# Kernel tuning notes

Measured on AMD Instinct MI355X. Metric: run time of the kernel, lower is better.

## Reference

```python
import jax, jax.numpy as jnp
import numpy as np

B, S, DM = 2, 2048, 1024  # batch, seq_len, model_dim
H, HD = 16, 64            # num_heads, head_dim (H*HD == DM)


def setup_inputs() -> dict:
    key = jax.random.key(0)
    ks = jax.random.split(key, 8)
    scale = 0.02
    return {
        "k": jax.random.normal(ks[0], (B, S, DM), jnp.float32),
        "q": jax.random.normal(ks[1], (B, S, DM), jnp.float32),
        "v": jax.random.normal(ks[2], (B, S, DM), jnp.float32),
        "Wk": jax.random.normal(ks[3], (DM, H * HD), jnp.float32) * scale,
        "bk": jnp.zeros((H * HD,), jnp.float32),
        "Wq": jax.random.normal(ks[4], (DM, H * HD), jnp.float32) * scale,
        "bq": jnp.zeros((H * HD,), jnp.float32),
        "Wv": jax.random.normal(ks[5], (DM, H * HD), jnp.float32) * scale,
        "bv": jnp.zeros((H * HD,), jnp.float32),
        "Wo": jax.random.normal(ks[6], (H * HD, DM), jnp.float32) * scale,
        "bo": jnp.zeros((DM,), jnp.float32),
    }


def reference(k, q, v, Wk, bk, Wq, bq, Wv, bv, Wo, bo):
    # QKV projections (Dense with bias)
    kp = (k @ Wk + bk).reshape(B, S, H, HD)
    qp = (q @ Wq + bq).reshape(B, S, H, HD)
    vp = (v @ Wv + bv).reshape(B, S, H, HD)
    # Faithful to original: scores indexed [b, key_c, h, query_q],
    # softmax over the QUERY axis, NO 1/sqrt(head_dim) scaling.
    scores = jnp.einsum('bchd,bqhd->bchq', kp, qp)
    attn = jax.nn.softmax(scores, axis=-1)
    out = jnp.einsum('bchq,bqhd->bchd', attn, vp)  # [B, S(keys), H, HD]
    out = out.reshape(B, S, H * HD)
    return out @ Wo + bo
```

## Files before the change

### kernel.cpp

```cpp
#include <hip/hip_runtime.h>
#include <hip/hip_bf16.h>
#include <stdint.h>
#include <stddef.h>


typedef __attribute__((ext_vector_type(4))) float f32x4;
typedef __attribute__((ext_vector_type(16))) float f32x16;
typedef __attribute__((ext_vector_type(8))) short s16x8;
typedef __attribute__((ext_vector_type(4))) unsigned int u32x4;
typedef __attribute__((ext_vector_type(4))) unsigned short u16x4;

#define DEV static __device__ __forceinline__

DEV unsigned short f2bf(float x) {
  unsigned int u = __float_as_uint(x);
  u += 0x7FFF + ((u >> 16) & 1);
  return (unsigned short)(u >> 16);
}
DEV f32x4 mfma16(s16x8 a, s16x8 b, f32x4 c) {
  return __builtin_amdgcn_mfma_f32_16x16x32_bf16(a, b, c, 0, 0, 0);
}
DEV f32x16 mfma32(s16x8 a, s16x8 b, f32x16 c) {
  return __builtin_amdgcn_mfma_f32_32x32x16_bf16(a, b, c, 0, 0, 0);
}
DEV f32x4 fzero() { f32x4 z; z[0]=0.f; z[1]=0.f; z[2]=0.f; z[3]=0.f; return z; }
DEV f32x16 fzero16() {
  f32x16 z;
#pragma unroll
  for (int i = 0; i < 16; ++i) z[i] = 0.f;
  return z;
}
DEV float fexp2(float x) { return __builtin_amdgcn_exp2f(x); }

DEV void gload_lds16(const unsigned short* g, unsigned short* l) {
  __builtin_amdgcn_global_load_lds(
      (const __attribute__((address_space(1))) unsigned int*)g,
      (__attribute__((address_space(3))) unsigned int*)l, 16, 0, 0);
}

#define CVTPK(dst, a, b) \
  asm("v_cvt_pk_bf16_f32 %0, %1, %2" : "=v"(dst) : "v"(a), "v"(b))
#define PSWAP(x, y) \
  asm("v_permlane32_swap_b32 %0, %1" : "+v"(x), "+v"(y))

struct PrepArgs {
  const float* x[3]; unsigned short* y[3];
  const float* W[4]; unsigned short* Wt[4];
};

__global__ __launch_bounds__(256) void prep_kernel(PrepArgs a) {
  __shared__ float t[32][33];
  const int plane = blockIdx.y;
  if (plane < 3) {
    const float* x = a.x[plane];
    unsigned short* y = a.y[plane];
    const int i = blockIdx.x * 256 + threadIdx.x;
    f32x4 v0 = ((const f32x4*)x)[2*i];
    f32x4 v1 = ((const f32x4*)x)[2*i + 1];
    u16x4 o0, o1;
#pragma unroll
    for (int j = 0; j < 4; ++j) { o0[j] = f2bf(v0[j]); o1[j] = f2bf(v1[j]); }
    ((u16x4*)y)[2*i] = o0;
    ((u16x4*)y)[2*i + 1] = o1;
  } else {
    if (blockIdx.x >= 1024) return;
    const float* W = a.W[plane - 3];
    unsigned short* Wt = a.Wt[plane - 3];
    const int n0 = (blockIdx.x & 31) * 32, k0 = (blockIdx.x >> 5) * 32;
    const int tx = threadIdx.x & 31, ty = threadIdx.x >> 5;
#pragma unroll
    for (int i = 0; i < 4; ++i)
      t[ty + i*8][tx] = W[(size_t)(k0 + ty + i*8) * 1024 + n0 + tx];
    __syncthreads();
#pragma unroll
    for (int i = 0; i < 4; ++i)
      Wt[(size_t)(n0 + ty + i*8) * 1024 + k0 + tx] = f2bf(t[tx][ty + i*8]);
  }
}

struct GemArgs {
  const unsigned short* A[3];
  const unsigned short* Wt[3];
  const float* bias[3];
  void* C[3];
  int mode[3];
  float scale[3];
};

template<int BM, int BN>
__global__ __launch_bounds__(256) void gemm_kernel(GemArgs g) {
  constexpr int MF = BM / 32;
  constexpr int NF = BN / 32;
  constexpr int NB = BN / 32;
  const int z = blockIdx.z;
  const unsigned short* A  = g.A[z];
  const unsigned short* Wt = g.Wt[z];
  const float* bias = g.bias[z];
  const int mode = g.mode[z];
  const float scale = g.scale[z];
  const int Fb = blockIdx.y * gridDim.x + blockIdx.x;
  const int chunk = gridDim.y >> 3;
  const int myi = (Fb & 7) * chunk + ((Fb >> 3) % chunk);
  const int nxi = (Fb >> 3) / chunk;
  const int m0 = myi * BM, n0 = nxi * BN;
  const int tid = threadIdx.x;
  const int lane = tid & 63, w = tid >> 6;
  const int wm = w >> 1, wn = w & 1;
  const int lg = lane >> 4, lr = lane & 15, lx = lr & 7;

  __shared__ __align__(16) unsigned short As[BM * 64];
  __shared__ __align__(16) unsigned short Bs[BN * 64];

  f32x4 acc[MF][NF];
#pragma unroll
  for (int i = 0; i < MF; ++i)
#pragma unroll
    for (int j = 0; j < NF; ++j) acc[i][j] = fzero();

  const int aStep = (mode == 2) ? 2048 * 64 : 64;
  const unsigned short* srcA[MF]; unsigned short* dstA[MF];
#pragma unroll
  for (int c = 0; c < MF; ++c) {
    int n = c*256 + tid, row = n >> 3, cg = (n & 7) ^ (row & 7);
    int s = m0 + row;
    size_t abase = (mode == 2)
        ? ((size_t)((s >> 11) * 16) * 2048 + (s & 2047)) * 64 + cg * 8
        : (size_t)s * 1024 + cg * 8;
    srcA[c] = A + abase;
    dstA[c] = &As[n * 8];
  }
  const unsigned short* srcB[NB]; unsigned short* dstB[NB];
#pragma unroll
  for (int c = 0; c < NB; ++c) {
    int n = c*256 + tid, row = n >> 3, cg = (n & 7) ^ (row & 7);
    srcB[c] = Wt + (size_t)(n0 + row) * 1024 + cg * 8;
    dstB[c] = &Bs[n * 8];
  }

  for (int it = 0; it < 16; ++it) {
    __syncthreads();
#pragma unroll
    for (int c = 0; c < MF; ++c) { gload_lds16(srcA[c], dstA[c]); srcA[c] += aStep; }
#pragma unroll
    for (int c = 0; c < NB; ++c) { gload_lds16(srcB[c], dstB[c]); srcB[c] += 64; }
    __syncthreads();

    s16x8 af[2][MF], bf[2][NF];
#pragma unroll
    for (int ks = 0; ks < 2; ++ks) {
#pragma unroll
      for (int mf = 0; mf < MF; ++mf) {
        int row = wm*(BM/2) + mf*16 + lr;
        af[ks][mf] = *(const s16x8*)&As[row*64 + ((ks*4 + lg) ^ lx) * 8];
      }
#pragma unroll
      for (int nf = 0; nf < NF; ++nf) {
        int row = wn*(BN/2) + nf*16 + lr;
        bf[ks][nf] = *(const s16x8*)&Bs[row*64 + ((ks*4 + lg) ^ lx) * 8];
      }
    }
#pragma unroll
    for (int mf = 0; mf < MF; ++mf)
#pragma unroll
      for (int nf = 0; nf < NF; ++nf) {
        acc[mf][nf] = mfma16(af[0][mf], bf[0][nf], acc[mf][nf]);
        acc[mf][nf] = mfma16(af[1][mf], bf[1][nf], acc[mf][nf]);
      }
  }

#pragma unroll
  for (int nf = 0; nf < NF; ++nf) {
    const int colg = n0 + wn*(BN/2) + nf*16 + lr;
    const float bi = bias[colg];
#pragma unroll
    for (int mf = 0; mf < MF; ++mf) {
      const int rowg0 = m0 + wm*(BM/2) + mf*16 + lg*4;
      if (mode == 0) {
        unsigned short* o = (unsigned short*)g.C[z];
#pragma unroll
        for (int r = 0; r < 4; ++r)
          o[(size_t)(rowg0 + r) * 1024 + colg] = f2bf((acc[mf][nf][r] + bi) * scale);
      } else if (mode == 1) {
        const int hh = colg >> 6, d = colg & 63;
        const int bb2 = rowg0 >> 11, s = rowg0 & 2047;
        u16x4 pk;
#pragma unroll
        for (int r = 0; r < 4; ++r) pk[r] = f2bf(acc[mf][nf][r] + bi);
        *(u16x4*)((unsigned short*)g.C[z] + ((size_t)((bb2*16 + hh)*64 + d)) * 2048 + s) = pk;
      } else {
        float* o = (float*)g.C[z];
#pragma unroll
        for (int r = 0; r < 4; ++r)
          o[(size_t)(rowg0 + r) * 1024 + colg] = acc[mf][nf][r] + bi;
      }
    }
  }
}

__global__ __launch_bounds__(256) void attn_kernel(
    const unsigned short* __restrict__ kp, const unsigned short* __restrict__ qp,
    const unsigned short* __restrict__ vpt, unsigned short* __restrict__ aout) {
  const int F = blockIdx.x;
  const int swz = (F & 7) * 64 + (F >> 3);
  const int bh = swz >> 4, cblk = swz & 15;
  const int b = bh >> 4, h = bh & 15;
  const int c0 = cblk * 128;
  const int tid = threadIdx.x, lane = tid & 63, w = tid >> 6;
  const int cg = w & 1, jg = w >> 1;
  const int ln = lane & 31, hh = lane >> 5;

  __shared__ __align__(16) unsigned short qa_lds[2][2][2048];
  __shared__ __align__(16) unsigned short vb_lds[2][2][2048];
  __shared__ float lbuf[2][2][64];

  const int srow = tid >> 3, sp = tid & 7, sl = sp ^ (srow & 7);
  const unsigned short* qsrc0 =
      qp + (size_t)(b*2048 + srow) * 1024 + h*64 + sl*8;
  const unsigned short* qsrc1 = qsrc0 + (size_t)1024 * 1024;
  const int sd = srow + 32*(sl >> 2), sjc = sl & 3;
  const unsigned short* vsrc0 =
      vpt + ((size_t)((b*16 + h)*64) + sd) * 2048 + sjc*8;
  const unsigned short* vsrc1 = vsrc0 + 1024;

  s16x8 kbA[4], kbB[4];
  {
    const unsigned short* krowA =
        kp + (size_t)(b*2048 + c0 + cg*64 + ln) * 1024 + h*64 + hh*8;
    const unsigned short* krowB = krowA + 32 * 1024;
#pragma unroll
    for (int s = 0; s < 4; ++s) {
      kbA[s] = *(const s16x8*)(krowA + s*16);
      kbB[s] = *(const s16x8*)(krowB + s*16);
    }
  }

  s16x8 onesA, onesB;
  {
    const short oa = (short)((ln < 16) ? 0x3F80 : 0);
    const short ob = (short)((ln < 16) ? 0 : 0x3F80);
#pragma unroll
    for (int i = 0; i < 8; ++i) { onesA[i] = oa; onesB[i] = ob; }
  }

  f32x16 accA0 = fzero16(), accA1 = fzero16();
  f32x16 accB0 = fzero16(), accB1 = fzero16();
  f32x16 lacc = fzero16();

  gload_lds16(qsrc0, &qa_lds[0][0][tid*8]);
  gload_lds16(qsrc1, &qa_lds[0][1][tid*8]);
  gload_lds16(vsrc0, &vb_lds[0][0][tid*8]);
  gload_lds16(vsrc1, &vb_lds[0][1][tid*8]);
  qsrc0 += 32*1024; qsrc1 += 32*1024; vsrc0 += 32; vsrc1 += 32;
  __syncthreads();

  for (int jt = 0; jt < 32; ++jt) {
    const int cur = jt & 1;
    if (jt + 1 < 32) {
      gload_lds16(qsrc0, &qa_lds[cur^1][0][tid*8]);
      gload_lds16(qsrc1, &qa_lds[cur^1][1][tid*8]);
      gload_lds16(vsrc0, &vb_lds[cur^1][0][tid*8]);
      gload_lds16(vsrc1, &vb_lds[cur^1][1][tid*8]);
      qsrc0 += 32*1024; qsrc1 += 32*1024; vsrc0 += 32; vsrc1 += 32;
    }

    s16x8 qa0, qa1, qa2, qa3;
    {
      const unsigned short* base = &qa_lds[cur][jg][0];
      qa0 = *(const s16x8*)&base[(ln*8 + ((0 + hh) ^ (ln & 7)))*8];
      qa1 = *(const s16x8*)&base[(ln*8 + ((2 + hh) ^ (ln & 7)))*8];
      qa2 = *(const s16x8*)&base[(ln*8 + ((4 + hh) ^ (ln & 7)))*8];
      qa3 = *(const s16x8*)&base[(ln*8 + ((6 + hh) ^ (ln & 7)))*8];
    }
    s16x8 vb0, vb1, vb2, vb3;
    {
      const unsigned short* base = &vb_lds[cur][jg][0];
      vb0 = *(const s16x8*)&base[(ln*8 + ((0 + hh) ^ (ln & 7)))*8];
      vb1 = *(const s16x8*)&base[(ln*8 + ((2 + hh) ^ (ln & 7)))*8];
      vb2 = *(const s16x8*)&base[(ln*8 + ((4 + hh) ^ (ln & 7)))*8];
      vb3 = *(const s16x8*)&base[(ln*8 + ((6 + hh) ^ (ln & 7)))*8];
    }

    f32x16 scA = fzero16(), scB = fzero16();
    __builtin_amdgcn_s_setprio(1);
    scA = mfma32(qa0, kbA[0], scA); scA = mfma32(qa1, kbA[1], scA);
    scA = mfma32(qa2, kbA[2], scA); scA = mfma32(qa3, kbA[3], scA);
    scB = mfma32(qa0, kbB[0], scB); scB = mfma32(qa1, kbB[1], scB);
    scB = mfma32(qa2, kbB[2], scB); scB = mfma32(qa3, kbB[3], scB);
    __builtin_amdgcn_s_setprio(0);

#define SOFTMAX_PV(SC, ONES, ACC0, ACC1)                                      \
  {                                                                           \
    _Pragma("unroll")                                                         \
    for (int r = 0; r < 16; ++r) SC[r] = fexp2(SC[r]);                        \
    unsigned int a0, a1, b0, b1;                                              \
    u32x4 wv; s16x8 pa0, pa1;                                                 \
    CVTPK(a0, SC[0], SC[1]);  CVTPK(b0, SC[4], SC[5]);  PSWAP(a0, b0);        \
    CVTPK(a1, SC[2], SC[3]);  CVTPK(b1, SC[6], SC[7]);  PSWAP(a1, b1);        \
    wv[0] = a0; wv[1] = a1; wv[2] = b0; wv[3] = b1;                           \
    pa0 = __builtin_bit_cast(s16x8, wv);                                      \
    CVTPK(a0, SC[8], SC[9]);  CVTPK(b0, SC[12], SC[13]); PSWAP(a0, b0);       \
    CVTPK(a1, SC[10], SC[11]); CVTPK(b1, SC[14], SC[15]); PSWAP(a1, b1);      \
    wv[0] = a0; wv[1] = a1; wv[2] = b0; wv[3] = b1;                           \
    pa1 = __builtin_bit_cast(s16x8, wv);                                      \
    __builtin_amdgcn_s_setprio(1);                                            \
    lacc = mfma32(ONES, pa0, lacc);                                           \
    lacc = mfma32(ONES, pa1, lacc);                                           \
    ACC0 = mfma32(vb0, pa0, ACC0);                                            \
    ACC0 = mfma32(vb1, pa1, ACC0);                                            \
    ACC1 = mfma32(vb2, pa0, ACC1);                                            \
    ACC1 = mfma32(vb3, pa1, ACC1);                                            \
    __builtin_amdgcn_s_setprio(0);                                            \
  }

    SOFTMAX_PV(scA, onesA, accA0, accA1);
    SOFTMAX_PV(scB, onesB, accB0, accB1);
#undef SOFTMAX_PV

    __syncthreads();
  }

  float lA = lacc[0], lB = lacc[8];

  float* mrg = cg ? (float*)&vb_lds[0][0][0] : (float*)&qa_lds[0][0][0];
  if (jg == 1) {
    lbuf[cg][0][lane] = lA; lbuf[cg][1][lane] = lB;
#pragma unroll
    for (int r = 0; r < 16; ++r) {
      mrg[(r)*64 + lane]      = accA0[r];
      mrg[(16 + r)*64 + lane] = accA1[r];
      mrg[(32 + r)*64 + lane] = accB0[r];
      mrg[(48 + r)*64 + lane] = accB1[r];
    }
  }
  __syncthreads();
  if (jg == 0) {
    lA += lbuf[cg][0][lane]; lB += lbuf[cg][1][lane];
#pragma unroll
    for (int r = 0; r < 16; ++r) {
      accA0[r] += mrg[(r)*64 + lane];
      accA1[r] += mrg[(16 + r)*64 + lane];
      accB0[r] += mrg[(32 + r)*64 + lane];
      accB1[r] += mrg[(48 + r)*64 + lane];
    }
    const float invA = 1.0f / lA, invB = 1.0f / lB;
    unsigned short* obaseA =
        aout + ((size_t)bh * 2048 + c0 + cg*64 + ln) * 64 + hh * 4;
    unsigned short* obaseB = obaseA + 32 * 64;
#pragma unroll
    for (int dt = 0; dt < 2; ++dt)
#pragma unroll
      for (int rq = 0; rq < 4; ++rq) {
        u16x4 pkA, pkB;
#pragma unroll
        for (int i = 0; i < 4; ++i) {
          const int reg = rq*4 + i;
          pkA[i] = f2bf(((dt == 0) ? accA0[reg] : accA1[reg]) * invA);
          pkB[i] = f2bf(((dt == 0) ? accB0[reg] : accB1[reg]) * invB);
        }
        *(u16x4*)(obaseA + dt*32 + rq*8) = pkA;
        *(u16x4*)(obaseB + dt*32 + rq*8) = pkB;
      }
  }
}

extern "C" void kernel_launch(void* const* d_in, const int* in_sizes, int n_in,
                              void* d_out, int out_size, void* d_ws, size_t ws_size,
                              hipStream_t stream) {
  (void)in_sizes; (void)n_in; (void)out_size; (void)ws_size;
  const float* k  = (const float*)d_in[0];
  const float* q  = (const float*)d_in[1];
  const float* v  = (const float*)d_in[2];
  const float* Wk = (const float*)d_in[3];
  const float* bk = (const float*)d_in[4];
  const float* Wq = (const float*)d_in[5];
  const float* bq = (const float*)d_in[6];
  const float* Wv = (const float*)d_in[7];
  const float* bv = (const float*)d_in[8];
  const float* Wo = (const float*)d_in[9];
  const float* bo = (const float*)d_in[10];

  char* ws = (char*)d_ws;
  const size_t MB = 1024 * 1024;
  unsigned short* Wkt = (unsigned short*)(ws + 0*MB);
  unsigned short* Wqt = (unsigned short*)(ws + 2*MB);
  unsigned short* Wvt = (unsigned short*)(ws + 4*MB);
  unsigned short* Wot = (unsigned short*)(ws + 6*MB);
  unsigned short* kp  = (unsigned short*)(ws + 8*MB);
  unsigned short* qp  = (unsigned short*)(ws + 16*MB);
  unsigned short* vpt = (unsigned short*)(ws + 24*MB);
  unsigned short* vc  = (unsigned short*)(ws + 32*MB);
  unsigned short* aoutb = (unsigned short*)(ws + 40*MB);
  unsigned short* kc = (unsigned short*)d_out;
  unsigned short* qc = (unsigned short*)((char*)d_out + 8*MB);

  PrepArgs pa;
  pa.x[0] = k; pa.x[1] = q; pa.x[2] = v;
  pa.y[0] = kc; pa.y[1] = qc; pa.y[2] = vc;
  pa.W[0] = Wk; pa.W[1] = Wq; pa.W[2] = Wv; pa.W[3] = Wo;
  pa.Wt[0] = Wkt; pa.Wt[1] = Wqt; pa.Wt[2] = Wvt; pa.Wt[3] = Wot;
  prep_kernel<<<dim3(2048, 7), 256, 0, stream>>>(pa);

  GemArgs gp;
  gp.A[0] = kc; gp.A[1] = qc; gp.A[2] = vc;
  gp.Wt[0] = Wkt; gp.Wt[1] = Wqt; gp.Wt[2] = Wvt;
  gp.bias[0] = bk; gp.bias[1] = bq; gp.bias[2] = bv;
  gp.C[0] = kp; gp.C[1] = qp; gp.C[2] = vpt;
  gp.mode[0] = 0; gp.mode[1] = 0; gp.mode[2] = 1;
  gp.scale[0] = 1.4426950408889634f;
  gp.scale[1] = 1.0f; gp.scale[2] = 1.0f;
  gemm_kernel<128, 128><<<dim3(8, 32, 3), 256, 0, stream>>>(gp);

  attn_kernel<<<dim3(512), 256, 0, stream>>>(kp, qp, vpt, aoutb);

  GemArgs gf;
  gf.A[0] = aoutb; gf.A[1] = aoutb; gf.A[2] = aoutb;
  gf.Wt[0] = Wot; gf.Wt[1] = Wot; gf.Wt[2] = Wot;
  gf.bias[0] = bo; gf.bias[1] = bo; gf.bias[2] = bo;
  gf.C[0] = d_out; gf.C[1] = d_out; gf.C[2] = d_out;
  gf.mode[0] = 2; gf.mode[1] = 2; gf.mode[2] = 2;
  gf.scale[0] = 1.0f; gf.scale[1] = 1.0f; gf.scale[2] = 1.0f;
  gemm_kernel<64, 64><<<dim3(16, 64, 1), 256, 0, stream>>>(gf);
}
```

Before: 123.0 us.

## Fuse fp32-to-bf16 activation conversion into QKV projection GEMM loads

Removes the separate pass that converted k, q, v activations to bf16 in the prep kernel. The QKV GEMM now reads fp32 activations directly through registers, packs them to bf16 with v_cvt_pk_bf16_f32 and writes them into LDS. This saves a full write and re-read of the converted activations and shrinks the prep launch. The A-tile loads now go through registers instead of async global-to-LDS loads, and each A tile reads twice as many bytes from global memory, since the fp32 values are refetched by the 8 column blocks instead of bf16 copies.

```diff
diff --git a/kernel.cpp b/kernel.cpp
--- a/kernel.cpp
+++ b/kernel.cpp
@@ -43,43 +43,25 @@
 #define PSWAP(x, y) \
   asm("v_permlane32_swap_b32 %0, %1" : "+v"(x), "+v"(y))
 
-struct PrepArgs {
-  const float* x[3]; unsigned short* y[3];
-  const float* W[4]; unsigned short* Wt[4];
-};
+struct PrepArgs { const float* W[4]; unsigned short* Wt[4]; };
 
 __global__ __launch_bounds__(256) void prep_kernel(PrepArgs a) {
   __shared__ float t[32][33];
-  const int plane = blockIdx.y;
-  if (plane < 3) {
-    const float* x = a.x[plane];
-    unsigned short* y = a.y[plane];
-    const int i = blockIdx.x * 256 + threadIdx.x;
-    f32x4 v0 = ((const f32x4*)x)[2*i];
-    f32x4 v1 = ((const f32x4*)x)[2*i + 1];
-    u16x4 o0, o1;
-#pragma unroll
-    for (int j = 0; j < 4; ++j) { o0[j] = f2bf(v0[j]); o1[j] = f2bf(v1[j]); }
-    ((u16x4*)y)[2*i] = o0;
-    ((u16x4*)y)[2*i + 1] = o1;
-  } else {
-    if (blockIdx.x >= 1024) return;
-    const float* W = a.W[plane - 3];
-    unsigned short* Wt = a.Wt[plane - 3];
-    const int n0 = (blockIdx.x & 31) * 32, k0 = (blockIdx.x >> 5) * 32;
-    const int tx = threadIdx.x & 31, ty = threadIdx.x >> 5;
-#pragma unroll
-    for (int i = 0; i < 4; ++i)
-      t[ty + i*8][tx] = W[(size_t)(k0 + ty + i*8) * 1024 + n0 + tx];
-    __syncthreads();
-#pragma unroll
-    for (int i = 0; i < 4; ++i)
-      Wt[(size_t)(n0 + ty + i*8) * 1024 + k0 + tx] = f2bf(t[tx][ty + i*8]);
-  }
+  const float* W = a.W[blockIdx.y];
+  unsigned short* Wt = a.Wt[blockIdx.y];
+  const int n0 = (blockIdx.x & 31) * 32, k0 = (blockIdx.x >> 5) * 32;
+  const int tx = threadIdx.x & 31, ty = threadIdx.x >> 5;
+#pragma unroll
+  for (int i = 0; i < 4; ++i)
+    t[ty + i*8][tx] = W[(size_t)(k0 + ty + i*8) * 1024 + n0 + tx];
+  __syncthreads();
+#pragma unroll
+  for (int i = 0; i < 4; ++i)
+    Wt[(size_t)(n0 + ty + i*8) * 1024 + k0 + tx] = f2bf(t[tx][ty + i*8]);
 }
 
 struct GemArgs {
-  const unsigned short* A[3];
+  const void* A[3];
   const unsigned short* Wt[3];
   const float* bias[3];
   void* C[3];
@@ -87,13 +69,11 @@
   float scale[3];
 };
 
-template<int BM, int BN>
+template<int BM, int BN, bool AF32>
 __global__ __launch_bounds__(256) void gemm_kernel(GemArgs g) {
   constexpr int MF = BM / 32;
   constexpr int NF = BN / 32;
-  constexpr int NB = BN / 32;
   const int z = blockIdx.z;
-  const unsigned short* A  = g.A[z];
   const unsigned short* Wt = g.Wt[z];
   const float* bias = g.bias[z];
   const int mode = g.mode[z];
@@ -117,21 +97,29 @@
 #pragma unroll
     for (int j = 0; j < NF; ++j) acc[i][j] = fzero();
 
-  const int aStep = (mode == 2) ? 2048 * 64 : 64;
-  const unsigned short* srcA[MF]; unsigned short* dstA[MF];
+  const float* srcAf[MF];
+  const unsigned short* srcA[MF];
+  unsigned short* dstA[MF];
 #pragma unroll
   for (int c = 0; c < MF; ++c) {
     int n = c*256 + tid, row = n >> 3, cg = (n & 7) ^ (row & 7);
     int s = m0 + row;
-    size_t abase = (mode == 2)
-        ? ((size_t)((s >> 11) * 16) * 2048 + (s & 2047)) * 64 + cg * 8
-        : (size_t)s * 1024 + cg * 8;
-    srcA[c] = A + abase;
+    if constexpr (AF32) {
+      srcAf[c] = (const float*)g.A[z] + (size_t)s * 1024 + cg * 8;
+      srcA[c] = nullptr;
+    } else {
+      size_t abase = (mode == 2)
+          ? ((size_t)((s >> 11) * 16) * 2048 + (s & 2047)) * 64 + cg * 8
+          : (size_t)s * 1024 + cg * 8;
+      srcA[c] = (const unsigned short*)g.A[z] + abase;
+      srcAf[c] = nullptr;
+    }
     dstA[c] = &As[n * 8];
   }
-  const unsigned short* srcB[NB]; unsigned short* dstB[NB];
-#pragma unroll
-  for (int c = 0; c < NB; ++c) {
+  const int aStep = (!AF32 && mode == 2) ? 2048 * 64 : 64;
+  const unsigned short* srcB[NF]; unsigned short* dstB[NF];
+#pragma unroll
+  for (int c = 0; c < NF; ++c) {
     int n = c*256 + tid, row = n >> 3, cg = (n & 7) ^ (row & 7);
     srcB[c] = Wt + (size_t)(n0 + row) * 1024 + cg * 8;
     dstB[c] = &Bs[n * 8];
@@ -139,10 +127,31 @@
 
   for (int it = 0; it < 16; ++it) {
     __syncthreads();
-#pragma unroll
-    for (int c = 0; c < MF; ++c) { gload_lds16(srcA[c], dstA[c]); srcA[c] += aStep; }
-#pragma unroll
-    for (int c = 0; c < NB; ++c) { gload_lds16(srcB[c], dstB[c]); srcB[c] += 64; }
+    if constexpr (AF32) {
+      f32x4 va[MF][2];
+#pragma unroll
+      for (int c = 0; c < MF; ++c) {
+        va[c][0] = *(const f32x4*)(srcAf[c]);
+        va[c][1] = *(const f32x4*)(srcAf[c] + 4);
+        srcAf[c] += 64;
+      }
+#pragma unroll
+      for (int c = 0; c < NF; ++c) { gload_lds16(srcB[c], dstB[c]); srcB[c] += 64; }
+#pragma unroll
+      for (int c = 0; c < MF; ++c) {
+        u32x4 pk;
+        CVTPK(pk[0], va[c][0][0], va[c][0][1]);
+        CVTPK(pk[1], va[c][0][2], va[c][0][3]);
+        CVTPK(pk[2], va[c][1][0], va[c][1][1]);
+        CVTPK(pk[3], va[c][1][2], va[c][1][3]);
+        *(u32x4*)dstA[c] = pk;
+      }
+    } else {
+#pragma unroll
+      for (int c = 0; c < MF; ++c) { gload_lds16(srcA[c], dstA[c]); srcA[c] += aStep; }
+#pragma unroll
+      for (int c = 0; c < NF; ++c) { gload_lds16(srcB[c], dstB[c]); srcB[c] += 64; }
+    }
     __syncthreads();
 
     s16x8 af[2][MF], bf[2][NF];
@@ -388,27 +397,22 @@
   unsigned short* kp  = (unsigned short*)(ws + 8*MB);
   unsigned short* qp  = (unsigned short*)(ws + 16*MB);
   unsigned short* vpt = (unsigned short*)(ws + 24*MB);
-  unsigned short* vc  = (unsigned short*)(ws + 32*MB);
   unsigned short* aoutb = (unsigned short*)(ws + 40*MB);
-  unsigned short* kc = (unsigned short*)d_out;
-  unsigned short* qc = (unsigned short*)((char*)d_out + 8*MB);
 
   PrepArgs pa;
-  pa.x[0] = k; pa.x[1] = q; pa.x[2] = v;
-  pa.y[0] = kc; pa.y[1] = qc; pa.y[2] = vc;
   pa.W[0] = Wk; pa.W[1] = Wq; pa.W[2] = Wv; pa.W[3] = Wo;
   pa.Wt[0] = Wkt; pa.Wt[1] = Wqt; pa.Wt[2] = Wvt; pa.Wt[3] = Wot;
-  prep_kernel<<<dim3(2048, 7), 256, 0, stream>>>(pa);
+  prep_kernel<<<dim3(1024, 4), 256, 0, stream>>>(pa);
 
   GemArgs gp;
-  gp.A[0] = kc; gp.A[1] = qc; gp.A[2] = vc;
+  gp.A[0] = k; gp.A[1] = q; gp.A[2] = v;
   gp.Wt[0] = Wkt; gp.Wt[1] = Wqt; gp.Wt[2] = Wvt;
   gp.bias[0] = bk; gp.bias[1] = bq; gp.bias[2] = bv;
   gp.C[0] = kp; gp.C[1] = qp; gp.C[2] = vpt;
   gp.mode[0] = 0; gp.mode[1] = 0; gp.mode[2] = 1;
   gp.scale[0] = 1.4426950408889634f;
   gp.scale[1] = 1.0f; gp.scale[2] = 1.0f;
-  gemm_kernel<128, 128><<<dim3(8, 32, 3), 256, 0, stream>>>(gp);
+  gemm_kernel<128, 128, true><<<dim3(8, 32, 3), 256, 0, stream>>>(gp);
 
   attn_kernel<<<dim3(512), 256, 0, stream>>>(kp, qp, vpt, aoutb);
 
@@ -419,5 +423,5 @@
   gf.C[0] = d_out; gf.C[1] = d_out; gf.C[2] = d_out;
   gf.mode[0] = 2; gf.mode[1] = 2; gf.mode[2] = 2;
   gf.scale[0] = 1.0f; gf.scale[1] = 1.0f; gf.scale[2] = 1.0f;
-  gemm_kernel<64, 64><<<dim3(16, 64, 1), 256, 0, stream>>>(gf);
-}
+  gemm_kernel<64, 64, false><<<dim3(16, 64, 1), 256, 0, stream>>>(gf);
+}
```

Result: no change. 125.2 us (+1.8%).
